# Kernel optimization log

Hardware: AMD Instinct MI355X
Metric: run time of the kernel (lower is better)

## Reference

```python
import jax, jax.numpy as jnp
import numpy as np
from jax import lax

EPS = 1e-8
DN = ('NCHW', 'OIHW', 'NCHW')


def setup_inputs() -> dict:
    key = jax.random.key(0)
    k1, k2 = jax.random.split(key)
    inputs = jax.random.normal(k1, (16, 3, 512, 512), dtype=jnp.float32)
    template = jax.random.normal(k2, (16, 3, 21, 21), dtype=jnp.float32)
    return {"inputs": inputs, "template": template}


def _normalize_template(template):
    # Z-normalize each (batch, channel) plane independently, then divide by
    # patch element count (matches NCC.__init__).
    B, C, th, tw = template.shape
    t = template.reshape(B, C, th * tw)
    t = t - jnp.mean(t, axis=-1, keepdims=True)
    t = t / (jnp.std(t, axis=-1, keepdims=True) + EPS)  # ddof=0 == unbiased=False
    return t.reshape(B, C, th, tw) / (th * tw)


def reference(inputs, template):
    B, C, H, W = inputs.shape
    th, tw = template.shape[2], template.shape[3]
    nt = _normalize_template(template)

    # Per-(b,c) depthwise cross-correlation (the grouped conv with eye-masked
    # weights is exactly a depthwise conv with per-sample filters).
    x = inputs.reshape(1, B * C, H, W)
    w = nt.reshape(B * C, 1, th, tw)
    res = lax.conv_general_dilated(x, w, (1, 1), 'VALID',
                                   dimension_numbers=DN,
                                   feature_group_count=B * C)
    res = res.reshape(B, C, res.shape[2], res.shape[3])  # (B,C,Hout,Wout)

    # Local (patch) std per channel via box filter (shared across batch).
    box = jnp.full((C, 1, th, tw), 1.0 / (th * tw), dtype=inputs.dtype)
    mean = lax.conv_general_dilated(inputs, box, (1, 1), 'VALID',
                                    dimension_numbers=DN, feature_group_count=C)
    mean_sq = lax.conv_general_dilated(inputs * inputs, box, (1, 1), 'VALID',
                                       dimension_numbers=DN, feature_group_count=C)
    std = jnp.sqrt(mean_sq - mean * mean + EPS)

    return res / (std + EPS)
```

## Files before the change

### kernel.cpp

```cpp
#include <hip/hip_runtime.h>
#include <math.h>

typedef __attribute__((ext_vector_type(8)))  short short8;
typedef __attribute__((ext_vector_type(16))) float f32x16;

#define NPLANE 48
#define H 512
#define W 512
#define TH 21
#define OH 492
#define OW 492
#define EPSF 1e-8f

#define STRIDE 168
#define SEG_ROWS 84

#define BONES_HOFF (4128768u / 2)

__device__ inline unsigned short f2bf(float f) {
    unsigned u = __float_as_uint(f);
    return (unsigned short)((u + 0x7FFFu + ((u >> 16) & 1u)) >> 16);
}
__device__ inline float bf2f(unsigned s) {
    return __uint_as_float(s << 16);
}
__device__ inline unsigned cvtpk(float lo, float hi) {
    unsigned r;
    asm("v_cvt_pk_bf16_f32 %0, %1, %2" : "=v"(r) : "v"(lo), "v"(hi));
    return r;
}

__global__ void build_b_kernel(const float* __restrict__ tpl,
                               unsigned short* __restrict__ ws16) {
    __shared__ float sm[2];
    const int plane = blockIdx.x;
    const float* t = tpl + plane * 441;
    const int tid = threadIdx.x;
    if (tid < 64) {
        float s = 0.f, s2 = 0.f;
        for (int k = tid; k < 441; k += 64) {
            float x = t[k];
            s += x; s2 += x * x;
        }
#pragma unroll
        for (int o = 32; o >= 1; o >>= 1) {
            s  += __shfl_down(s, o);
            s2 += __shfl_down(s2, o);
        }
        if (tid == 0) {
            float mean = s / 441.f;
            float var = fmaxf(s2 / 441.f - mean * mean, 0.f);
            sm[0] = mean;
            sm[1] = 1.f / ((sqrtf(var) + EPSF) * 441.f);
        }
    }
    __syncthreads();
    const float mean = sm[0], scale = sm[1];

    unsigned short* bc = ws16 + (size_t)plane * 43008;
    for (int i = tid; i < 43008; i += 256) {
        int j = i & 7, lane = (i >> 3) & 63, s = (i >> 9) & 3, u = i >> 11;
        int k = ((lane >> 5) << 3) + j, n = lane & 31;
        int v = 16 * s + k - n;
        float val = (v >= 0 && v < TH) ? (t[u * 21 + v] - mean) * scale : 0.f;
        bc[i] = f2bf(val);
    }
    if (plane == 0) {
        unsigned short* bo = ws16 + BONES_HOFF;
        const unsigned short one = f2bf(1.f);
        for (int i = tid; i < 2048; i += 256) {
            int j = i & 7, lane = (i >> 3) & 63, s = (i >> 9) & 3;
            int k = ((lane >> 5) << 3) + j, n = lane & 31;
            int v = 16 * s + k - n;
            bo[i] = (v >= 0 && v < TH) ? one : (unsigned short)0;
        }
    }
}

__global__ __launch_bounds__(256, 4) void ncc_fused_kernel(
    const float* __restrict__ in, const unsigned short* __restrict__ ws16,
    float* __restrict__ out) {
    __shared__ short seg[SEG_ROWS * STRIDE];
    __shared__ short vbuf[32 * STRIDE];

    const int plane = blockIdx.z;
    const int x0 = blockIdx.x * 128;
    const int y0 = blockIdx.y * 64;
    const int tid = threadIdx.x;
    const int lane = tid & 63;
    const int tr = (tid >> 6) & 1;
    const int tc = tid >> 7;
    const float* src = in + (size_t)plane * H * W;

    for (int i = tid; i < SEG_ROWS * 20; i += 256) {
        int row = i / 20, s8 = i - row * 20;
        int gy = y0 + row, gx = x0 + s8 * 8;
        if (gy < H && gx + 7 < W) {
            float4 a = *(const float4*)(src + gy * W + gx);
            float4 b = *(const float4*)(src + gy * W + gx + 4);
            uint4 v;
            v.x = cvtpk(a.x, a.y);
            v.y = cvtpk(a.z, a.w);
            v.z = cvtpk(b.x, b.y);
            v.w = cvtpk(b.z, b.w);
            *(uint4*)&seg[row * STRIDE + s8 * 8] = v;
        } else {
            short8 val;
#pragma unroll
            for (int e = 0; e < 8; ++e) {
                float xv = (gy < H && gx + e < W) ? src[gy * W + gx + e] : 0.f;
                val[e] = (short)f2bf(xv);
            }
            *(short8*)&seg[row * STRIDE + s8 * 8] = val;
        }
    }
    __syncthreads();

    const int m = lane & 31;
    const int half = lane >> 5;
    const int abase = (tr * 32 + m) * STRIDE + tc * 64 + half * 8;
    const int vbase = m * STRIDE + tc * 64 + half * 8;
    const unsigned short* bc = ws16 + (size_t)plane * 43008 + lane * 8;

    f32x16 acc[2];
#pragma unroll
    for (int t = 0; t < 2; ++t)
#pragma unroll
        for (int e = 0; e < 16; ++e) acc[t][e] = 0.f;

    auto corr_step = [&](int u, short8* bf) {
        short8 af[6];
#pragma unroll
        for (int g = 0; g < 6; ++g)
            af[g] = *(const short8*)&seg[abase + u * STRIDE + g * 16];
#pragma unroll
        for (int t = 0; t < 2; ++t)
#pragma unroll
            for (int s = 0; s < 4; ++s)
                acc[t] = __builtin_amdgcn_mfma_f32_32x32x16_bf16(
                    af[2 * t + s], bf[s], acc[t], 0, 0, 0);
    };

    short8 bA[4], bB[4];
#pragma unroll
    for (int s = 0; s < 4; ++s)
        bA[s] = *(const short8*)(bc + s * 512);

    for (int u = 0; u < TH - 1; u += 2) {
#pragma unroll
        for (int s = 0; s < 4; ++s)
            bB[s] = *(const short8*)(bc + ((u + 1) * 4 + s) * 512);
        corr_step(u, bA);
#pragma unroll
        for (int s = 0; s < 4; ++s)
            bA[s] = *(const short8*)(bc + ((u + 2) * 4 + s) * 512);
        corr_step(u + 1, bB);
    }
    corr_step(TH - 1, bA);

    auto vpass = [&](int Hh, bool sq) {
        if (tid < 160) {
            const int sub = (tid >= 80) ? 16 : 0;
            const int c2 = (tid % 80) * 2;
            const int base = Hh * 32 + sub;
            float s0 = 0.f, s1 = 0.f;
#pragma unroll
            for (int r = 0; r < 20; ++r) {
                unsigned p = *(const unsigned*)&seg[(base + r) * STRIDE + c2];
                float a = bf2f(p & 0xffffu), b = bf2f(p >> 16);
                if (sq) { s0 = fmaf(a, a, s0); s1 = fmaf(b, b, s1); }
                else    { s0 += a; s1 += b; }
            }
            for (int yb = 0; yb < 16; yb += 8) {
                unsigned pin[8], pout[8];
#pragma unroll
                for (int r = 0; r < 8; ++r) {
                    pin[r]  = *(const unsigned*)
                        &seg[(base + yb + r + 20) * STRIDE + c2];
                    pout[r] = *(const unsigned*)
                        &seg[(base + yb + r) * STRIDE + c2];
                }
#pragma unroll
                for (int r = 0; r < 8; ++r) {
                    float a = bf2f(pin[r] & 0xffffu), b = bf2f(pin[r] >> 16);
                    if (sq) { s0 = fmaf(a, a, s0); s1 = fmaf(b, b, s1); }
                    else    { s0 += a; s1 += b; }
                    *(unsigned*)&vbuf[(sub + yb + r) * STRIDE + c2] =
                        cvtpk(s0, s1);
                    float c = bf2f(pout[r] & 0xffffu), d = bf2f(pout[r] >> 16);
                    if (sq) { s0 = fmaf(-c, c, s0); s1 = fmaf(-d, d, s1); }
                    else    { s0 -= c; s1 -= d; }
                }
            }
        }
    };

    f32x16 aS[2];
    auto box = [&](f32x16* dst) {
        const unsigned short* bo16 = ws16 + BONES_HOFF + lane * 8;
        short8 bn[4];
#pragma unroll
        for (int s = 0; s < 4; ++s)
            bn[s] = *(const short8*)(bo16 + s * 512);
#pragma unroll
        for (int t = 0; t < 2; ++t) {
#pragma unroll
            for (int e = 0; e < 16; ++e) dst[t][e] = 0.f;
#pragma unroll
            for (int s = 0; s < 4; ++s) {
                short8 vf = *(const short8*)&vbuf[vbase + (2 * t + s) * 16];
                dst[t] = __builtin_amdgcn_mfma_f32_32x32x16_bf16(
                    vf, bn[s], dst[t], 0, 0, 0);
            }
        }
    };

    auto finish = [&]() {
        const unsigned short* bo16 = ws16 + BONES_HOFF + lane * 8;
        short8 bn[4];
#pragma unroll
        for (int s = 0; s < 4; ++s)
            bn[s] = *(const short8*)(bo16 + s * 512);
        const float invn = 1.f / 441.f;
        float* outp = out + (size_t)plane * OH * OW;
#pragma unroll
        for (int t = 0; t < 2; ++t) {
            f32x16 q;
#pragma unroll
            for (int e = 0; e < 16; ++e) q[e] = 0.f;
#pragma unroll
            for (int s = 0; s < 4; ++s) {
                short8 qf = *(const short8*)&vbuf[vbase + (2 * t + s) * 16];
                q = __builtin_amdgcn_mfma_f32_32x32x16_bf16(qf, bn[s], q,
                                                            0, 0, 0);
            }
            const int gx = x0 + tc * 64 + t * 32 + m;
            if (gx < OW) {
#pragma unroll
                for (int r = 0; r < 16; ++r) {
                    int gy = y0 + tr * 32 + (r & 3) + ((r >> 2) << 3) + half * 4;
                    if (gy < OH) {
                        float mean = aS[t][r] * invn;
                        float msq = q[r] * invn;
                        float sd = sqrtf(msq - mean * mean + EPSF);
                        outp[(size_t)gy * OW + gx] = acc[t][r] / (sd + EPSF);
                    }
                }
            }
        }
    };

    vpass(0, false);
    __syncthreads();
    if (tr == 0) box(aS);
    __syncthreads();
    vpass(1, false);
    __syncthreads();
    if (tr == 1) box(aS);
    __syncthreads();
    vpass(0, true);
    __syncthreads();
    if (tr == 0) finish();
    __syncthreads();
    vpass(1, true);
    __syncthreads();
    if (tr == 1) finish();
}

extern "C" void kernel_launch(void* const* d_in, const int* in_sizes, int n_in,
                              void* d_out, int out_size, void* d_ws,
                              size_t ws_size, hipStream_t stream) {
    const float* inputs = (const float*)d_in[0];
    const float* tmpl = (const float*)d_in[1];
    float* out = (float*)d_out;
    unsigned short* ws16 = (unsigned short*)d_ws;

    build_b_kernel<<<NPLANE, 256, 0, stream>>>(tmpl, ws16);
    ncc_fused_kernel<<<dim3(4, 8, NPLANE), 256, 0, stream>>>(inputs, ws16, out);
}
```

Baseline: 165.8 us.

## Use 512-thread blocks with one 32x32 tile per wave and single-pass box sums

```diff
diff --git a/kernel.cpp b/kernel.cpp
--- a/kernel.cpp
+++ b/kernel.cpp
@@ -77,22 +77,23 @@
     }
 }
 
-__global__ __launch_bounds__(256, 4) void ncc_fused_kernel(
+__global__ __launch_bounds__(512, 6) void ncc_fused_kernel(
     const float* __restrict__ in, const unsigned short* __restrict__ ws16,
     float* __restrict__ out) {
     __shared__ short seg[SEG_ROWS * STRIDE];
-    __shared__ short vbuf[32 * STRIDE];
+    __shared__ short vbuf[64 * STRIDE];
 
     const int plane = blockIdx.z;
     const int x0 = blockIdx.x * 128;
     const int y0 = blockIdx.y * 64;
     const int tid = threadIdx.x;
     const int lane = tid & 63;
-    const int tr = (tid >> 6) & 1;
-    const int tc = tid >> 7;
+    const int wid = tid >> 6;
+    const int tr = wid & 1;
+    const int tc = wid >> 1;
     const float* src = in + (size_t)plane * H * W;
 
-    for (int i = tid; i < SEG_ROWS * 20; i += 256) {
+    for (int i = tid; i < SEG_ROWS * 20; i += 512) {
         int row = i / 20, s8 = i - row * 20;
         int gy = y0 + row, gx = x0 + s8 * 8;
         if (gy < H && gx + 7 < W) {
@@ -118,27 +119,22 @@
 
     const int m = lane & 31;
     const int half = lane >> 5;
-    const int abase = (tr * 32 + m) * STRIDE + tc * 64 + half * 8;
-    const int vbase = m * STRIDE + tc * 64 + half * 8;
+    const int abase = (tr * 32 + m) * STRIDE + tc * 32 + half * 8;
     const unsigned short* bc = ws16 + (size_t)plane * 43008 + lane * 8;
 
-    f32x16 acc[2];
-#pragma unroll
-    for (int t = 0; t < 2; ++t)
-#pragma unroll
-        for (int e = 0; e < 16; ++e) acc[t][e] = 0.f;
+    f32x16 acc;
+#pragma unroll
+    for (int e = 0; e < 16; ++e) acc[e] = 0.f;
 
     auto corr_step = [&](int u, short8* bf) {
-        short8 af[6];
-#pragma unroll
-        for (int g = 0; g < 6; ++g)
-            af[g] = *(const short8*)&seg[abase + u * STRIDE + g * 16];
-#pragma unroll
-        for (int t = 0; t < 2; ++t)
-#pragma unroll
-            for (int s = 0; s < 4; ++s)
-                acc[t] = __builtin_amdgcn_mfma_f32_32x32x16_bf16(
-                    af[2 * t + s], bf[s], acc[t], 0, 0, 0);
+        short8 af[4];
+#pragma unroll
+        for (int s = 0; s < 4; ++s)
+            af[s] = *(const short8*)&seg[abase + u * STRIDE + s * 16];
+#pragma unroll
+        for (int s = 0; s < 4; ++s)
+            acc = __builtin_amdgcn_mfma_f32_32x32x16_bf16(af[s], bf[s], acc,
+                                                          0, 0, 0);
     };
 
     short8 bA[4], bB[4];
@@ -158,11 +154,17 @@
     }
     corr_step(TH - 1, bA);
 
-    auto vpass = [&](int Hh, bool sq) {
-        if (tid < 160) {
-            const int sub = (tid >= 80) ? 16 : 0;
-            const int c2 = (tid % 80) * 2;
-            const int base = Hh * 32 + sub;
+    const unsigned short* bo16 = ws16 + BONES_HOFF + lane * 8;
+    short8 bones[4];
+#pragma unroll
+    for (int s = 0; s < 4; ++s)
+        bones[s] = *(const short8*)(bo16 + s * 512);
+
+    auto vpass = [&](bool sq) {
+        if (tid < 320) {
+            const int q = tid / 80;
+            const int c2 = (tid - q * 80) * 2;
+            const int base = q * 16;
             float s0 = 0.f, s1 = 0.f;
 #pragma unroll
             for (int r = 0; r < 20; ++r) {
@@ -171,6 +173,7 @@
                 if (sq) { s0 = fmaf(a, a, s0); s1 = fmaf(b, b, s1); }
                 else    { s0 += a; s1 += b; }
             }
+#pragma unroll
             for (int yb = 0; yb < 16; yb += 8) {
                 unsigned pin[8], pout[8];
 #pragma unroll
@@ -185,7 +188,7 @@
                     float a = bf2f(pin[r] & 0xffffu), b = bf2f(pin[r] >> 16);
                     if (sq) { s0 = fmaf(a, a, s0); s1 = fmaf(b, b, s1); }
                     else    { s0 += a; s1 += b; }
-                    *(unsigned*)&vbuf[(sub + yb + r) * STRIDE + c2] =
+                    *(unsigned*)&vbuf[(base + yb + r) * STRIDE + c2] =
                         cvtpk(s0, s1);
                     float c = bf2f(pout[r] & 0xffffu), d = bf2f(pout[r] >> 16);
                     if (sq) { s0 = fmaf(-c, c, s0); s1 = fmaf(-d, d, s1); }
@@ -195,76 +198,49 @@
         }
     };
 
-    f32x16 aS[2];
-    auto box = [&](f32x16* dst) {
-        const unsigned short* bo16 = ws16 + BONES_HOFF + lane * 8;
-        short8 bn[4];
-#pragma unroll
-        for (int s = 0; s < 4; ++s)
-            bn[s] = *(const short8*)(bo16 + s * 512);
-#pragma unroll
-        for (int t = 0; t < 2; ++t) {
-#pragma unroll
-            for (int e = 0; e < 16; ++e) dst[t][e] = 0.f;
-#pragma unroll
-            for (int s = 0; s < 4; ++s) {
-                short8 vf = *(const short8*)&vbuf[vbase + (2 * t + s) * 16];
-                dst[t] = __builtin_amdgcn_mfma_f32_32x32x16_bf16(
-                    vf, bn[s], dst[t], 0, 0, 0);
-            }
-        }
-    };
-
-    auto finish = [&]() {
-        const unsigned short* bo16 = ws16 + BONES_HOFF + lane * 8;
-        short8 bn[4];
-#pragma unroll
-        for (int s = 0; s < 4; ++s)
-            bn[s] = *(const short8*)(bo16 + s * 512);
-        const float invn = 1.f / 441.f;
-        float* outp = out + (size_t)plane * OH * OW;
-#pragma unroll
-        for (int t = 0; t < 2; ++t) {
-            f32x16 q;
-#pragma unroll
-            for (int e = 0; e < 16; ++e) q[e] = 0.f;
-#pragma unroll
-            for (int s = 0; s < 4; ++s) {
-                short8 qf = *(const short8*)&vbuf[vbase + (2 * t + s) * 16];
-                q = __builtin_amdgcn_mfma_f32_32x32x16_bf16(qf, bn[s], q,
-                                                            0, 0, 0);
-            }
-            const int gx = x0 + tc * 64 + t * 32 + m;
-            if (gx < OW) {
-#pragma unroll
-                for (int r = 0; r < 16; ++r) {
-                    int gy = y0 + tr * 32 + (r & 3) + ((r >> 2) << 3) + half * 4;
-                    if (gy < OH) {
-                        float mean = aS[t][r] * invn;
-                        float msq = q[r] * invn;
-                        float sd = sqrtf(msq - mean * mean + EPSF);
-                        outp[(size_t)gy * OW + gx] = acc[t][r] / (sd + EPSF);
-                    }
-                }
-            }
-        }
-    };
-
-    vpass(0, false);
-    __syncthreads();
-    if (tr == 0) box(aS);
-    __syncthreads();
-    vpass(1, false);
-    __syncthreads();
-    if (tr == 1) box(aS);
-    __syncthreads();
-    vpass(0, true);
-    __syncthreads();
-    if (tr == 0) finish();
-    __syncthreads();
-    vpass(1, true);
-    __syncthreads();
-    if (tr == 1) finish();
+    vpass(false);
+    __syncthreads();
+
+    f32x16 aS;
+#pragma unroll
+    for (int e = 0; e < 16; ++e) aS[e] = 0.f;
+#pragma unroll
+    for (int s = 0; s < 4; ++s) {
+        short8 vf = *(const short8*)&vbuf[abase + s * 16];
+        aS = __builtin_amdgcn_mfma_f32_32x32x16_bf16(vf, bones[s], aS,
+                                                     0, 0, 0);
+    }
+    __syncthreads();
+
+    vpass(true);
+    __syncthreads();
+
+    f32x16 aQ;
+#pragma unroll
+    for (int e = 0; e < 16; ++e) aQ[e] = 0.f;
+#pragma unroll
+    for (int s = 0; s < 4; ++s) {
+        short8 qf = *(const short8*)&vbuf[abase + s * 16];
+        aQ = __builtin_amdgcn_mfma_f32_32x32x16_bf16(qf, bones[s], aQ,
+                                                     0, 0, 0);
+    }
+
+    const float invn = 1.f / 441.f;
+    float* outp = out + (size_t)plane * OH * OW;
+    const int gx = x0 + tc * 32 + m;
+    if (gx < OW) {
+#pragma unroll
+        for (int r = 0; r < 16; ++r) {
+            int gy = y0 + tr * 32 + (r & 3) + ((r >> 2) << 3) + half * 4;
+            if (gy < OH) {
+                float mean = aS[r] * invn;
+                float msq = aQ[r] * invn;
+                float var = fmaf(-mean, mean, msq) + EPSF;
+                outp[(size_t)gy * OW + gx] =
+                    acc[r] * __builtin_amdgcn_rsqf(var);
+            }
+        }
+    }
 }
 
 extern "C" void kernel_launch(void* const* d_in, const int* in_sizes, int n_in,
@@ -276,5 +252,5 @@
     unsigned short* ws16 = (unsigned short*)d_ws;
 
     build_b_kernel<<<NPLANE, 256, 0, stream>>>(tmpl, ws16);
-    ncc_fused_kernel<<<dim3(4, 8, NPLANE), 256, 0, stream>>>(inputs, ws16, out);
-}
+    ncc_fused_kernel<<<dim3(4, 8, NPLANE), 512, 0, stream>>>(inputs, ws16, out);
+}
```

Result: no change. 167.2 us (+0.9%).

## Merge vertical passes into full-height buffer, cut barriers, triple-buffer template loads

Applied to the files above, without the earlier changes.

```diff
diff --git a/kernel.cpp b/kernel.cpp
--- a/kernel.cpp
+++ b/kernel.cpp
@@ -21,13 +21,14 @@
     unsigned u = __float_as_uint(f);
     return (unsigned short)((u + 0x7FFFu + ((u >> 16) & 1u)) >> 16);
 }
-__device__ inline float bf2f(unsigned s) {
-    return __uint_as_float(s << 16);
-}
 __device__ inline unsigned cvtpk(float lo, float hi) {
     unsigned r;
     asm("v_cvt_pk_bf16_f32 %0, %1, %2" : "=v"(r) : "v"(lo), "v"(hi));
     return r;
+}
+__device__ inline float unpk_lo(unsigned p) { return __uint_as_float(p << 16); }
+__device__ inline float unpk_hi(unsigned p) {
+    return __uint_as_float(p & 0xffff0000u);
 }
 
 __global__ void build_b_kernel(const float* __restrict__ tpl,
@@ -77,11 +78,11 @@
     }
 }
 
-__global__ __launch_bounds__(256, 4) void ncc_fused_kernel(
+__global__ __launch_bounds__(256, 3) void ncc_fused_kernel(
     const float* __restrict__ in, const unsigned short* __restrict__ ws16,
     float* __restrict__ out) {
     __shared__ short seg[SEG_ROWS * STRIDE];
-    __shared__ short vbuf[32 * STRIDE];
+    __shared__ short vbuf[64 * STRIDE];
 
     const int plane = blockIdx.z;
     const int x0 = blockIdx.x * 128;
@@ -119,7 +120,6 @@
     const int m = lane & 31;
     const int half = lane >> 5;
     const int abase = (tr * 32 + m) * STRIDE + tc * 64 + half * 8;
-    const int vbase = m * STRIDE + tc * 64 + half * 8;
     const unsigned short* bc = ws16 + (size_t)plane * 43008 + lane * 8;
 
     f32x16 acc[2];
@@ -134,60 +134,66 @@
         for (int g = 0; g < 6; ++g)
             af[g] = *(const short8*)&seg[abase + u * STRIDE + g * 16];
 #pragma unroll
-        for (int t = 0; t < 2; ++t)
-#pragma unroll
-            for (int s = 0; s < 4; ++s)
+        for (int s = 0; s < 4; ++s)
+#pragma unroll
+            for (int t = 0; t < 2; ++t)
                 acc[t] = __builtin_amdgcn_mfma_f32_32x32x16_bf16(
                     af[2 * t + s], bf[s], acc[t], 0, 0, 0);
     };
 
-    short8 bA[4], bB[4];
+    auto bload = [&](short8* dst, int u) {
+#pragma unroll
+        for (int s = 0; s < 4; ++s)
+            dst[s] = *(const short8*)(bc + (u * 4 + s) * 512);
+    };
+
+    short8 b0[4], b1[4], b2[4];
+    bload(b0, 0); bload(b1, 1); bload(b2, 2);
+    for (int u = 0; u < TH; u += 3) {
+        corr_step(u, b0);
+        bload(b0, (u + 3 < TH) ? u + 3 : 0);
+        corr_step(u + 1, b1);
+        bload(b1, (u + 4 < TH) ? u + 4 : 0);
+        corr_step(u + 2, b2);
+        bload(b2, (u + 5 < TH) ? u + 5 : 0);
+    }
+
+    const unsigned short* bo16 = ws16 + BONES_HOFF + lane * 8;
+    short8 bones[4];
 #pragma unroll
     for (int s = 0; s < 4; ++s)
-        bA[s] = *(const short8*)(bc + s * 512);
-
-    for (int u = 0; u < TH - 1; u += 2) {
-#pragma unroll
-        for (int s = 0; s < 4; ++s)
-            bB[s] = *(const short8*)(bc + ((u + 1) * 4 + s) * 512);
-        corr_step(u, bA);
-#pragma unroll
-        for (int s = 0; s < 4; ++s)
-            bA[s] = *(const short8*)(bc + ((u + 2) * 4 + s) * 512);
-        corr_step(u + 1, bB);
-    }
-    corr_step(TH - 1, bA);
-
-    auto vpass = [&](int Hh, bool sq) {
+        bones[s] = *(const short8*)(bo16 + s * 512);
+
+    auto vpass = [&](bool sq) {
         if (tid < 160) {
-            const int sub = (tid >= 80) ? 16 : 0;
+            const int hr = (tid >= 80) ? 32 : 0;
             const int c2 = (tid % 80) * 2;
-            const int base = Hh * 32 + sub;
             float s0 = 0.f, s1 = 0.f;
 #pragma unroll
             for (int r = 0; r < 20; ++r) {
-                unsigned p = *(const unsigned*)&seg[(base + r) * STRIDE + c2];
-                float a = bf2f(p & 0xffffu), b = bf2f(p >> 16);
+                unsigned p = *(const unsigned*)&seg[(hr + r) * STRIDE + c2];
+                float a = unpk_lo(p), b = unpk_hi(p);
                 if (sq) { s0 = fmaf(a, a, s0); s1 = fmaf(b, b, s1); }
                 else    { s0 += a; s1 += b; }
             }
-            for (int yb = 0; yb < 16; yb += 8) {
+#pragma unroll
+            for (int yy = 0; yy < 32; yy += 8) {
                 unsigned pin[8], pout[8];
 #pragma unroll
                 for (int r = 0; r < 8; ++r) {
                     pin[r]  = *(const unsigned*)
-                        &seg[(base + yb + r + 20) * STRIDE + c2];
+                        &seg[(hr + yy + r + 20) * STRIDE + c2];
                     pout[r] = *(const unsigned*)
-                        &seg[(base + yb + r) * STRIDE + c2];
+                        &seg[(hr + yy + r) * STRIDE + c2];
                 }
 #pragma unroll
                 for (int r = 0; r < 8; ++r) {
-                    float a = bf2f(pin[r] & 0xffffu), b = bf2f(pin[r] >> 16);
+                    float a = unpk_lo(pin[r]), b = unpk_hi(pin[r]);
                     if (sq) { s0 = fmaf(a, a, s0); s1 = fmaf(b, b, s1); }
                     else    { s0 += a; s1 += b; }
-                    *(unsigned*)&vbuf[(sub + yb + r) * STRIDE + c2] =
+                    *(unsigned*)&vbuf[(hr + yy + r) * STRIDE + c2] =
                         cvtpk(s0, s1);
-                    float c = bf2f(pout[r] & 0xffffu), d = bf2f(pout[r] >> 16);
+                    float c = unpk_lo(pout[r]), d = unpk_hi(pout[r]);
                     if (sq) { s0 = fmaf(-c, c, s0); s1 = fmaf(-d, d, s1); }
                     else    { s0 -= c; s1 -= d; }
                 }
@@ -195,76 +201,63 @@
         }
     };
 
+    vpass(false);
+    __syncthreads();
+
     f32x16 aS[2];
-    auto box = [&](f32x16* dst) {
-        const unsigned short* bo16 = ws16 + BONES_HOFF + lane * 8;
-        short8 bn[4];
-#pragma unroll
-        for (int s = 0; s < 4; ++s)
-            bn[s] = *(const short8*)(bo16 + s * 512);
+#pragma unroll
+    for (int t = 0; t < 2; ++t)
+#pragma unroll
+        for (int e = 0; e < 16; ++e) aS[t][e] = 0.f;
+#pragma unroll
+    for (int s = 0; s < 4; ++s)
 #pragma unroll
         for (int t = 0; t < 2; ++t) {
-#pragma unroll
-            for (int e = 0; e < 16; ++e) dst[t][e] = 0.f;
-#pragma unroll
-            for (int s = 0; s < 4; ++s) {
-                short8 vf = *(const short8*)&vbuf[vbase + (2 * t + s) * 16];
-                dst[t] = __builtin_amdgcn_mfma_f32_32x32x16_bf16(
-                    vf, bn[s], dst[t], 0, 0, 0);
-            }
-        }
-    };
-
-    auto finish = [&]() {
-        const unsigned short* bo16 = ws16 + BONES_HOFF + lane * 8;
-        short8 bn[4];
-#pragma unroll
-        for (int s = 0; s < 4; ++s)
-            bn[s] = *(const short8*)(bo16 + s * 512);
-        const float invn = 1.f / 441.f;
-        float* outp = out + (size_t)plane * OH * OW;
+            short8 vf = *(const short8*)&vbuf[abase + (2 * t + s) * 16];
+            aS[t] = __builtin_amdgcn_mfma_f32_32x32x16_bf16(vf, bones[s],
+                                                            aS[t], 0, 0, 0);
+        }
+    __syncthreads();
+
+    vpass(true);
+    __syncthreads();
+
+    f32x16 aQ[2];
+#pragma unroll
+    for (int t = 0; t < 2; ++t)
+#pragma unroll
+        for (int e = 0; e < 16; ++e) aQ[t][e] = 0.f;
+#pragma unroll
+    for (int s = 0; s < 4; ++s)
 #pragma unroll
         for (int t = 0; t < 2; ++t) {
-            f32x16 q;
-#pragma unroll
-            for (int e = 0; e < 16; ++e) q[e] = 0.f;
-#pragma unroll
-            for (int s = 0; s < 4; ++s) {
-                short8 qf = *(const short8*)&vbuf[vbase + (2 * t + s) * 16];
-                q = __builtin_amdgcn_mfma_f32_32x32x16_bf16(qf, bn[s], q,
-                                                            0, 0, 0);
-            }
-            const int gx = x0 + tc * 64 + t * 32 + m;
-            if (gx < OW) {
-#pragma unroll
-                for (int r = 0; r < 16; ++r) {
-                    int gy = y0 + tr * 32 + (r & 3) + ((r >> 2) << 3) + half * 4;
-                    if (gy < OH) {
-                        float mean = aS[t][r] * invn;
-                        float msq = q[r] * invn;
-                        float sd = sqrtf(msq - mean * mean + EPSF);
-                        outp[(size_t)gy * OW + gx] = acc[t][r] / (sd + EPSF);
-                    }
-                }
-            }
-        }
-    };
-
-    vpass(0, false);
-    __syncthreads();
-    if (tr == 0) box(aS);
-    __syncthreads();
-    vpass(1, false);
-    __syncthreads();
-    if (tr == 1) box(aS);
-    __syncthreads();
-    vpass(0, true);
-    __syncthreads();
-    if (tr == 0) finish();
-    __syncthreads();
-    vpass(1, true);
-    __syncthreads();
-    if (tr == 1) finish();
+            short8 qf = *(const short8*)&vbuf[abase + (2 * t + s) * 16];
+            aQ[t] = __builtin_amdgcn_mfma_f32_32x32x16_bf16(qf, bones[s],
+                                                            aQ[t], 0, 0, 0);
+        }
+
+    const float invn = 1.f / 441.f;
+    float* outp = out + (size_t)plane * OH * OW;
+#pragma unroll
+    for (int t = 0; t < 2; ++t) {
+        float vout[16];
+#pragma unroll
+        for (int r = 0; r < 16; ++r) {
+            float mean = aS[t][r] * invn;
+            float msq = aQ[t][r] * invn;
+            float var = fmaf(-mean, mean, msq) + EPSF;
+            vout[r] = acc[t][r] * __builtin_amdgcn_rsqf(var);
+        }
+        const int gx = x0 + tc * 64 + t * 32 + m;
+        if (gx < OW) {
+#pragma unroll
+            for (int r = 0; r < 16; ++r) {
+                int gy = y0 + tr * 32 + (r & 3) + ((r >> 2) << 3) + half * 4;
+                if (gy < OH)
+                    outp[(size_t)gy * OW + gx] = vout[r];
+            }
+        }
+    }
 }
 
 extern "C" void kernel_launch(void* const* d_in, const int* in_sizes, int n_in,
```

Measured after the change: 161.7 us. 2.4% less time.
